# Kernel optimization log

Hardware: AMD Instinct MI355X
Metric: run time of the kernel (lower is better)

## Reference

```python
import jax, jax.numpy as jnp
import numpy as np


def log_g(x):
    # log of g(x) = where(x>=0, x+0.5, sigmoid(x)), computed stably in log space
    return jnp.where(x >= 0.0, jnp.log(jax.nn.relu(x) + 0.5), -jax.nn.softplus(-x))


def setup_inputs() -> dict:
    key = jax.random.key(0)
    k1, k2, k3 = jax.random.split(key, 3)
    B, T, D = 4, 4096, 512
    D_inner = 4 * D  # expansion_factor = 4.0
    x = jax.random.normal(k1, (B, T, D), dtype=jnp.float32)
    # torch Linear weights: W_hg [2*D_inner, D], W_out [D, D_inner]
    W_hg = jax.random.normal(k2, (2 * D_inner, D), dtype=jnp.float32) * 0.02
    b_hg = jnp.zeros((2 * D_inner,), dtype=jnp.float32)
    W_out = jax.random.normal(k3, (D, D_inner), dtype=jnp.float32) * 0.02
    b_out = jnp.zeros((D,), dtype=jnp.float32)
    return {"x": x, "W_hg": W_hg, "b_hg": b_hg, "W_out": W_out, "b_out": b_out}


def reference(x, W_hg, b_hg, W_out, b_out):
    # x: [B, T, D]
    hg = jnp.einsum('btd,ed->bte', x, W_hg) + b_hg          # [B, T, 2*D_inner]
    hidden, gate = jnp.split(hg, 2, axis=-1)                # each [B, T, D_inner]

    log_coeffs = -jax.nn.softplus(gate)                     # log a_t = log sigmoid(-gate)... = log(1-z)
    log_z = -jax.nn.softplus(-gate)                         # log z_t = log sigmoid(gate)
    log_values = log_z + log_g(hidden)                      # log b_t

    # pad one step at front of time axis (prev_hidden=None path: padded log value 0)
    pad = ((0, 0), (1, 0), (0, 0))
    log_coeffs_p = jnp.pad(log_coeffs, pad)                 # [B, T+1, D_inner]
    log_values_p = jnp.pad(log_values, pad)

    # Heinsen log-space associative scan
    a_star = jnp.cumsum(log_coeffs_p, axis=1)
    log_h = a_star + jax.lax.cumlogsumexp(log_values_p - a_star, axis=1)
    h = jnp.exp(log_h)[:, 1:, :]                            # [B, T, D_inner]

    out = jnp.einsum('bte,de->btd', h, W_out) + b_out       # [B, T, D]
    return out
```

## Files before the change

### kernel.cpp

```cpp
#include <hip/hip_runtime.h>
#include <hip/hip_bf16.h>
#include <type_traits>

#define B_   4
#define T_   4096
#define D_   512
#define E_   2048
#define M_   (B_*T_)
#define N1_  (2*E_)
#define K1_  D_
#define N2_  D_
#define K2_  E_
#define CT_  128
#define NC_  (T_/CT_)

typedef __attribute__((ext_vector_type(8))) short short8_t;
typedef __attribute__((ext_vector_type(4))) float f32x4;

__device__ inline unsigned short f2bf(float f){
  unsigned u = __float_as_uint(f);
  u += 0x7fffu + ((u >> 16) & 1u);
  return (unsigned short)(u >> 16);
}
__device__ inline float bf2f(unsigned h){ return __uint_as_float(h << 16); }
__device__ inline float fast_rcp(float x){
  float r; asm("v_rcp_f32 %0, %1" : "=v"(r) : "v"(x)); return r;
}
__device__ inline unsigned pk_bf16(float lo, float hi){
  unsigned r; asm("v_cvt_pk_bf16_f32 %0, %1, %2" : "=v"(r) : "v"(lo), "v"(hi)); return r;
}

template<int I, int N, typename F>
__device__ __forceinline__ void sfor(F&& f){
  if constexpr (I < N) { f(std::integral_constant<int, I>{}); sfor<I + 1, N>(f); }
}

__global__ __launch_bounds__(256) void conv_f32_bf16_x4(const float* __restrict__ in,
                                                        short* __restrict__ out, int n4){
  int i = blockIdx.x * 256 + threadIdx.x;
  if (i >= n4) return;
  float4 v = ((const float4*)in)[i];
  short4 o;
  o.x = (short)f2bf(v.x); o.y = (short)f2bf(v.y);
  o.z = (short)f2bf(v.z); o.w = (short)f2bf(v.w);
  ((short4*)out)[i] = o;
}

__global__ __launch_bounds__(128) void conv_whg(const float* __restrict__ W,
                                                short* __restrict__ Wp){
  int r = blockIdx.x;
  int e = ((r >> 6) << 5) + (r & 31);
  int orig = e + ((r >> 5) & 1) * E_;
  float4 v = ((const float4*)(W + (size_t)orig * K1_))[threadIdx.x];
  short4 o;
  o.x = (short)f2bf(v.x); o.y = (short)f2bf(v.y);
  o.z = (short)f2bf(v.z); o.w = (short)f2bf(v.w);
  ((short4*)(Wp + (size_t)r * K1_))[threadIdx.x] = o;
}

template<int EPI, int KK>
__global__ __launch_bounds__(256, 2)
void gemm_db(const short* __restrict__ A, const short* __restrict__ Bmat,
             const float* __restrict__ bias,
             unsigned* __restrict__ ab_out,
             float* __restrict__ c_out, int ldc)
{
  __shared__ short As[2][128 * 64];
  __shared__ short Bs[2][128 * 64];
  constexpr int NT = KK / 64;

  const int tid  = threadIdx.x;
  const int lane = tid & 63;
  const int w    = tid >> 6;
  const int wr   = (w >> 1) * 64;
  const int wc   = (w & 1) * 64;

  const int gx  = gridDim.x;
  const int nwg = gx * gridDim.y;
  const int lin = blockIdx.y * gx + blockIdx.x;
  const int cp  = nwg >> 3;
  const int xcd = lin & 7;
  const int q   = lin >> 3;
  const int TW  = (gx < 8) ? gx : 8;
  const int TH  = 64 / TW;
  const int tile = q >> 6, s = q & 63;
  const int tpb  = gx / TW;
  const int band = tile / tpb, tb = tile - band * tpb;
  const int browL = band * TH + s / TW;
  const int bcol  = (tb * TW + (s % TW)) * 128;
  const int brow  = (xcd * (cp / gx) + browL) * 128;

  f32x4 acc[4][4];
  #pragma unroll
  for (int m = 0; m < 4; ++m)
    #pragma unroll
    for (int n = 0; n < 4; ++n) acc[m][n] = (f32x4){0.f, 0.f, 0.f, 0.f};

  const int srow = lane >> 3;
  const int scol = ((lane & 7) ^ srow) * 8;
  const int l15  = lane & 15;
  const int kh   = (lane >> 4) * 8;
  const int sw   = (l15 & 7) << 3;

  const short* ga[4]; const short* gb[4];
  #pragma unroll
  for (int i = 0; i < 4; ++i) {
    const int rr = (w * 4 + i) * 8 + srow;
    ga[i] = A    + (size_t)(brow + rr) * KK + scol;
    gb[i] = Bmat + (size_t)(bcol + rr) * KK + scol;
  }

  auto stage = [&](auto CUR, auto TT) {
    constexpr int cb = decltype(CUR)::value;
    constexpr int kt = decltype(TT)::value * 64;
    #pragma unroll
    for (int i = 0; i < 4; ++i) {
      __builtin_amdgcn_global_load_lds(
          (const __attribute__((address_space(1))) void*)(ga[i] + kt),
          (__attribute__((address_space(3))) void*)&As[cb][(w * 4 + i) * 512], 16, 0, 0);
      __builtin_amdgcn_global_load_lds(
          (const __attribute__((address_space(1))) void*)(gb[i] + kt),
          (__attribute__((address_space(3))) void*)&Bs[cb][(w * 4 + i) * 512], 16, 0, 0);
    }
  };
  auto comp = [&](auto CUR) {
    constexpr int cb = decltype(CUR)::value;
    #pragma unroll
    for (int kk = 0; kk < 64; kk += 32) {
      short8_t afr[4], bfr[4];
      #pragma unroll
      for (int m = 0; m < 4; ++m)
        afr[m] = *(const short8_t*)&As[cb][(wr + m * 16 + l15) * 64 + ((kk + kh) ^ sw)];
      #pragma unroll
      for (int n = 0; n < 4; ++n)
        bfr[n] = *(const short8_t*)&Bs[cb][(wc + n * 16 + l15) * 64 + ((kk + kh) ^ sw)];
      #pragma unroll
      for (int m = 0; m < 4; ++m)
        #pragma unroll
        for (int n = 0; n < 4; ++n)
          acc[m][n] = __builtin_amdgcn_mfma_f32_16x16x32_bf16(afr[m], bfr[n], acc[m][n], 0, 0, 0);
    }
  };

  stage(std::integral_constant<int, 0>{}, std::integral_constant<int, 0>{});
  __syncthreads();

  sfor<0, NT>([&](auto TT) {
    constexpr int t   = decltype(TT)::value;
    constexpr int cur = t & 1;
    if constexpr (t + 1 < NT)
      stage(std::integral_constant<int, cur ^ 1>{}, std::integral_constant<int, t + 1>{});
    comp(std::integral_constant<int, cur>{});
    if constexpr (t + 1 < NT) __syncthreads();
  });

  const int r4 = (lane >> 4) * 4;
  if constexpr (EPI == 0) {
    const int ebase = (bcol + wc) >> 1;
    #pragma unroll
    for (int m = 0; m < 4; ++m) {
      const int row = brow + wr + m * 16 + r4;
      #pragma unroll
      for (int n = 0; n < 2; ++n) {
        const int e = ebase + n * 16 + l15;
        const float bh = bias[e];
        const float bg = bias[E_ + e];
        #pragma unroll
        for (int j = 0; j < 4; ++j) {
          float hh = acc[m][n][j]     + bh;
          float gg = acc[m][n + 2][j] + bg;
          float r  = fast_rcp(1.f + __expf(-fabsf(gg)));
          float z  = (gg >= 0.f) ? r : 1.f - r;
          float a  = 1.f - z;
          float gf = (hh >= 0.f) ? (hh + 0.5f) : fast_rcp(1.f + __expf(-hh));
          float bb = z * gf;
          __builtin_nontemporal_store(pk_bf16(a, bb),
                                      &ab_out[(size_t)(row + j) * E_ + e]);
        }
      }
    }
  } else {
    #pragma unroll
    for (int m = 0; m < 4; ++m) {
      #pragma unroll
      for (int n = 0; n < 4; ++n) {
        const int row = brow + wr + m * 16 + r4;
        const int col = bcol + wc + n * 16 + l15;
        #pragma unroll
        for (int j = 0; j < 4; ++j)
          __builtin_nontemporal_store(acc[m][n][j] + bias[col],
                                      &c_out[(size_t)(row + j) * ldc + col]);
      }
    }
  }
}

__global__ __launch_bounds__(256) void scan_chunk(const unsigned* __restrict__ ab,
                                                  float* __restrict__ Ac,
                                                  float* __restrict__ Bc){
  const int c = blockIdx.x;
  const int e = (blockIdx.y * 256 + threadIdx.x) * 4;
  const int b = blockIdx.z;
  size_t base = (((size_t)b * T_ + (size_t)c * CT_) * E_ + e) >> 2;
  const uint4* abv = (const uint4*)ab;
  float A0=1.f,A1=1.f,A2=1.f,A3=1.f, H0=0.f,H1=0.f,H2=0.f,H3=0.f;
  #pragma unroll 4
  for (int t = 0; t < CT_; ++t) {
    uint4 wv = abv[base + (size_t)t * (E_ / 4)];
    float a0=bf2f(wv.x&0xffffu), b0=bf2f(wv.x>>16);
    float a1=bf2f(wv.y&0xffffu), b1=bf2f(wv.y>>16);
    float a2=bf2f(wv.z&0xffffu), b2=bf2f(wv.z>>16);
    float a3=bf2f(wv.w&0xffffu), b3=bf2f(wv.w>>16);
    H0=fmaf(a0,H0,b0); H1=fmaf(a1,H1,b1); H2=fmaf(a2,H2,b2); H3=fmaf(a3,H3,b3);
    A0*=a0; A1*=a1; A2*=a2; A3*=a3;
  }
  size_t ci = (((size_t)b * NC_ + c) * E_ + e) >> 2;
  ((float4*)Ac)[ci] = (float4){A0,A1,A2,A3};
  ((float4*)Bc)[ci] = (float4){H0,H1,H2,H3};
}

__global__ __launch_bounds__(256) void scan_carry(const float* __restrict__ Ac,
                                                  const float* __restrict__ Bc,
                                                  float* __restrict__ Hc){
  int idx = blockIdx.x * 256 + threadIdx.x;
  int b = idx >> 11;
  int e = idx & (E_ - 1);
  float H = 1.f;
  for (int c = 0; c < NC_; ++c) {
    size_t ci = ((size_t)b * NC_ + c) * E_ + e;
    float A = Ac[ci], Bv = Bc[ci];
    Hc[ci] = H;
    H = fmaf(A, H, Bv);
  }
}

__global__ __launch_bounds__(256) void scan_final(const unsigned* __restrict__ ab,
                                                  const float* __restrict__ Hc,
                                                  short* __restrict__ h){
  const int c = blockIdx.x;
  const int e = (blockIdx.y * 256 + threadIdx.x) * 4;
  const int b = blockIdx.z;
  size_t base = (((size_t)b * T_ + (size_t)c * CT_) * E_ + e) >> 2;
  const uint4* abv = (const uint4*)ab;
  float4 Hv = ((const float4*)Hc)[(((size_t)b * NC_ + c) * E_ + e) >> 2];
  float H0=Hv.x, H1=Hv.y, H2=Hv.z, H3=Hv.w;
  short4* hv = (short4*)h;
  #pragma unroll 4
  for (int t = 0; t < CT_; ++t) {
    uint4 wv = abv[base + (size_t)t * (E_ / 4)];
    H0 = fmaf(bf2f(wv.x&0xffffu), H0, bf2f(wv.x>>16));
    H1 = fmaf(bf2f(wv.y&0xffffu), H1, bf2f(wv.y>>16));
    H2 = fmaf(bf2f(wv.z&0xffffu), H2, bf2f(wv.z>>16));
    H3 = fmaf(bf2f(wv.w&0xffffu), H3, bf2f(wv.w>>16));
    short4 o;
    o.x=(short)f2bf(H0); o.y=(short)f2bf(H1); o.z=(short)f2bf(H2); o.w=(short)f2bf(H3);
    hv[base + (size_t)t * (E_ / 4)] = o;
  }
}

extern "C" void kernel_launch(void* const* d_in, const int* in_sizes, int n_in,
                              void* d_out, int out_size, void* d_ws, size_t ws_size,
                              hipStream_t stream)
{
  const float* x     = (const float*)d_in[0];
  const float* W_hg  = (const float*)d_in[1];
  const float* b_hg  = (const float*)d_in[2];
  const float* W_out = (const float*)d_in[3];
  const float* b_out = (const float*)d_in[4];
  float* out = (float*)d_out;

  char* p = (char*)d_ws;
  auto carve = [&](size_t bytes) -> char* {
    char* q = p; p += (bytes + 255) & ~(size_t)255; return q;
  };
  short*    xb   = (short*)   carve((size_t)M_ * K1_ * 2);
  short*    Wp   = (short*)   carve((size_t)N1_ * K1_ * 2);
  short*    Wo   = (short*)   carve((size_t)N2_ * K2_ * 2);
  unsigned* ab   = (unsigned*)carve((size_t)M_ * E_ * 4);
  short*    hbuf = (short*)   carve((size_t)M_ * E_ * 2);
  float*    Ac   = (float*)   carve((size_t)B_ * NC_ * E_ * 4);
  float*    Bc   = (float*)   carve((size_t)B_ * NC_ * E_ * 4);
  float*    Hc   = (float*)   carve((size_t)B_ * NC_ * E_ * 4);

  conv_f32_bf16_x4<<<(M_ * K1_ / 4 + 255) / 256, 256, 0, stream>>>(x, xb, M_ * K1_ / 4);
  conv_whg<<<N1_, 128, 0, stream>>>(W_hg, Wp);
  conv_f32_bf16_x4<<<(N2_ * K2_ / 4 + 255) / 256, 256, 0, stream>>>(W_out, Wo, N2_ * K2_ / 4);

  gemm_db<0, K1_><<<dim3(N1_ / 128, M_ / 128), 256, 0, stream>>>(xb, Wp, b_hg, ab, nullptr, 0);

  scan_chunk<<<dim3(NC_, E_ / 1024, B_), 256, 0, stream>>>(ab, Ac, Bc);
  scan_carry<<<(B_ * E_) / 256, 256, 0, stream>>>(Ac, Bc, Hc);
  scan_final<<<dim3(NC_, E_ / 1024, B_), 256, 0, stream>>>(ab, Hc, hbuf);

  gemm_db<1, K2_><<<dim3(N2_ / 128, M_ / 128), 256, 0, stream>>>(hbuf, Wo, b_out, nullptr, out, N2_);
}
```

Before: 317.0 us.

## Load GEMM A fragments directly from global into registers, drop A LDS staging

The A operand no longer goes through shared memory. Each wave loads its MFMA fragments straight from global memory into registers each k-step, while B keeps the double-buffered LDS path. This halves LDS usage, which allows occupancy to rise to 3 workgroups per CU, and removes the LDS reads for A. In exchange, A fragments are not shared between the two waves that need the same rows, so global and L2 traffic for A doubles. The global loads are also issued synchronously right before compute with no prefetch, so their latency may be exposed. Nontemporal stores in both epilogues are replaced by plain stores.

```diff
diff --git a/kernel.cpp b/kernel.cpp
--- a/kernel.cpp
+++ b/kernel.cpp
@@ -59,13 +59,12 @@
 }
 
 template<int EPI, int KK>
-__global__ __launch_bounds__(256, 2)
+__global__ __launch_bounds__(256, 3)
 void gemm_db(const short* __restrict__ A, const short* __restrict__ Bmat,
              const float* __restrict__ bias,
              unsigned* __restrict__ ab_out,
              float* __restrict__ c_out, int ldc)
 {
-  __shared__ short As[2][128 * 64];
   __shared__ short Bs[2][128 * 64];
   constexpr int NT = KK / 64;
 
@@ -102,35 +101,40 @@
   const int kh   = (lane >> 4) * 8;
   const int sw   = (l15 & 7) << 3;
 
-  const short* ga[4]; const short* gb[4];
+  const short* gA[4];
   #pragma unroll
-  for (int i = 0; i < 4; ++i) {
-    const int rr = (w * 4 + i) * 8 + srow;
-    ga[i] = A    + (size_t)(brow + rr) * KK + scol;
-    gb[i] = Bmat + (size_t)(bcol + rr) * KK + scol;
-  }
-
-  auto stage = [&](auto CUR, auto TT) {
+  for (int m = 0; m < 4; ++m)
+    gA[m] = A + (size_t)(brow + wr + m * 16 + l15) * KK + kh;
+
+  const short* gb[4];
+  #pragma unroll
+  for (int i = 0; i < 4; ++i)
+    gb[i] = Bmat + (size_t)(bcol + (w * 4 + i) * 8 + srow) * KK + scol;
+
+  short8_t af[4][2];
+  auto loadA = [&](auto TT) {
+    constexpr int kt = decltype(TT)::value * 64;
+    #pragma unroll
+    for (int m = 0; m < 4; ++m) {
+      af[m][0] = *(const short8_t*)(gA[m] + kt);
+      af[m][1] = *(const short8_t*)(gA[m] + kt + 32);
+    }
+  };
+  auto stageB = [&](auto CUR, auto TT) {
     constexpr int cb = decltype(CUR)::value;
     constexpr int kt = decltype(TT)::value * 64;
     #pragma unroll
-    for (int i = 0; i < 4; ++i) {
-      __builtin_amdgcn_global_load_lds(
-          (const __attribute__((address_space(1))) void*)(ga[i] + kt),
-          (__attribute__((address_space(3))) void*)&As[cb][(w * 4 + i) * 512], 16, 0, 0);
+    for (int i = 0; i < 4; ++i)
       __builtin_amdgcn_global_load_lds(
           (const __attribute__((address_space(1))) void*)(gb[i] + kt),
           (__attribute__((address_space(3))) void*)&Bs[cb][(w * 4 + i) * 512], 16, 0, 0);
-    }
   };
   auto comp = [&](auto CUR) {
     constexpr int cb = decltype(CUR)::value;
     #pragma unroll
-    for (int kk = 0; kk < 64; kk += 32) {
-      short8_t afr[4], bfr[4];
-      #pragma unroll
-      for (int m = 0; m < 4; ++m)
-        afr[m] = *(const short8_t*)&As[cb][(wr + m * 16 + l15) * 64 + ((kk + kh) ^ sw)];
+    for (int kx = 0; kx < 2; ++kx) {
+      const int kk = kx * 32;
+      short8_t bfr[4];
       #pragma unroll
       for (int n = 0; n < 4; ++n)
         bfr[n] = *(const short8_t*)&Bs[cb][(wc + n * 16 + l15) * 64 + ((kk + kh) ^ sw)];
@@ -138,18 +142,19 @@
       for (int m = 0; m < 4; ++m)
         #pragma unroll
         for (int n = 0; n < 4; ++n)
-          acc[m][n] = __builtin_amdgcn_mfma_f32_16x16x32_bf16(afr[m], bfr[n], acc[m][n], 0, 0, 0);
-    }
-  };
-
-  stage(std::integral_constant<int, 0>{}, std::integral_constant<int, 0>{});
+          acc[m][n] = __builtin_amdgcn_mfma_f32_16x16x32_bf16(af[m][kx], bfr[n], acc[m][n], 0, 0, 0);
+    }
+  };
+
+  stageB(std::integral_constant<int, 0>{}, std::integral_constant<int, 0>{});
   __syncthreads();
 
   sfor<0, NT>([&](auto TT) {
     constexpr int t   = decltype(TT)::value;
     constexpr int cur = t & 1;
+    loadA(TT);
     if constexpr (t + 1 < NT)
-      stage(std::integral_constant<int, cur ^ 1>{}, std::integral_constant<int, t + 1>{});
+      stageB(std::integral_constant<int, cur ^ 1>{}, std::integral_constant<int, t + 1>{});
     comp(std::integral_constant<int, cur>{});
     if constexpr (t + 1 < NT) __syncthreads();
   });
@@ -174,8 +179,7 @@
           float a  = 1.f - z;
           float gf = (hh >= 0.f) ? (hh + 0.5f) : fast_rcp(1.f + __expf(-hh));
           float bb = z * gf;
-          __builtin_nontemporal_store(pk_bf16(a, bb),
-                                      &ab_out[(size_t)(row + j) * E_ + e]);
+          ab_out[(size_t)(row + j) * E_ + e] = pk_bf16(a, bb);
         }
       }
     }
@@ -188,8 +192,7 @@
         const int col = bcol + wc + n * 16 + l15;
         #pragma unroll
         for (int j = 0; j < 4; ++j)
-          __builtin_nontemporal_store(acc[m][n][j] + bias[col],
-                                      &c_out[(size_t)(row + j) * ldc + col]);
+          c_out[(size_t)(row + j) * ldc + col] = acc[m][n][j] + bias[col];
       }
     }
   }
```

New measurement: 392.8 us. 23.9% more time.
